# Performance work log

Measured on AMD Instinct MI355X. Metric: run time of the kernel, lower is better.

Reference implementation:

```python
import jax, jax.numpy as jnp
import numpy as np

EPS = 1e-8      # torch CosineSimilarity eps (clamps norms)
GAMMA = 0.5
RANK = 2        # hardcoded in the module; rank-1 = 1 negative per sample


def _cos_dist(a, b):
    # angular distance sqrt(2*(1-cos)) along last dim, torch-style eps on norms
    na = jnp.clip(jnp.linalg.norm(a, axis=-1), EPS)
    nb = jnp.clip(jnp.linalg.norm(b, axis=-1), EPS)
    sim = jnp.sum(a * b, axis=-1) / (na * nb)
    return jnp.sqrt(jnp.maximum(2.0 * (1.0 - sim), 1e-12))


def setup_inputs() -> dict:
    key = jax.random.key(0)
    k1, k2, k3 = jax.random.split(key, 3)
    B, D, V = 4096, 512, 50000
    return {
        "input": jax.random.normal(k1, (B, D), dtype=jnp.float32),
        "target": jax.random.normal(k2, (B, D), dtype=jnp.float32),
        "veclist": jax.random.normal(k3, (V, D), dtype=jnp.float32),
    }


def reference(input, target, veclist):
    B = input.shape[0]
    # distance to the true target per sample: [B]
    d_pos = _cos_dist(input, target)

    # brute-force angular kNN over veclist (replaces the Annoy index):
    # max cosine similarity == min angular distance
    inn = input / jnp.clip(jnp.linalg.norm(input, axis=-1, keepdims=True), EPS)
    vnn = veclist / jnp.clip(jnp.linalg.norm(veclist, axis=-1, keepdims=True), EPS)
    sims = inn @ vnn.T                                # [B, V] -- the big GEMM
    _, top_idx = jax.lax.top_k(sims, RANK)            # [B, 2]

    vec0 = veclist[top_idx[:, 0]]                     # [B, D]
    vec1 = veclist[top_idx[:, 1]]                     # [B, D]
    # skip the neighbor if it is exactly the target vector (original `torch.eq` check)
    eq0 = jnp.all(vec0 == target, axis=-1)            # [B]
    neg = jnp.where(eq0[:, None], vec1, vec0)         # [B, D]

    d_neg = _cos_dist(input, neg)                     # [B]
    # original builds sample_dist of shape [rank]=[2] (gamma_vec bug repeats gamma
    # `rank` times), with both entries identical -> sum of positives = 2*relu(margin)
    margin = GAMMA + d_pos - d_neg                    # [B]
    cost = jnp.sum(RANK * jnp.maximum(margin, 0.0))
    return cost / B
```

## Files before the change

### kernel.cpp

```cpp
#include <hip/hip_runtime.h>
#include <hip/hip_bf16.h>
#include <hip/hip_fp8.h>
#include <math.h>

#define B_ROWS 4096
#define DIMS   512
#define V_ROWS 50000
#define V_PAD  50048
#define NTILES 391
#define NT_PAD 392
#define MTILES 32
#define BKB    128
#define NROWS_ALL 54144
#define EPSF   1e-8f
#define QSCALE 64.0f
#define SCALE1 0x7F7F7F7F

typedef float f32x4 __attribute__((ext_vector_type(4)));
typedef int   i32x4 __attribute__((ext_vector_type(4)));
typedef int   i32x8 __attribute__((ext_vector_type(8)));
typedef unsigned long long u64;

__device__ __forceinline__ unsigned int pk4_fp8(float a, float b, float c, float d) {
#if __has_builtin(__builtin_amdgcn_cvt_pk_fp8_f32)
  int w = __builtin_amdgcn_cvt_pk_fp8_f32(a, b, 0, false);
  w = __builtin_amdgcn_cvt_pk_fp8_f32(c, d, w, true);
  return (unsigned int)w;
#else
  __hip_fp8_e4m3 qa(a), qb(b), qc(c), qd(d);
  return (unsigned int)qa.__x | ((unsigned int)qb.__x << 8) |
         ((unsigned int)qc.__x << 16) | ((unsigned int)qd.__x << 24);
#endif
}

__device__ __forceinline__ void lds_load16(const void* g, void* l) {
  __builtin_amdgcn_global_load_lds(
      (const __attribute__((address_space(1))) void*)g,
      (__attribute__((address_space(3))) void*)l, 16, 0, 0);
}

__device__ __forceinline__ u64 pack_key(float v, int col) {
  unsigned int u = __float_as_uint(v);
  unsigned int s = u ^ ((unsigned int)((int)u >> 31) | 0x80000000u);
  return ((u64)s << 32) | (unsigned int)(~col);
}
__device__ __forceinline__ int key_col(u64 k) {
  return (int)(~(unsigned int)k);
}
__device__ __forceinline__ void kmerge(u64& k0, u64& k1, u64 a0, u64 a1) {
  bool bt = a0 > k0;
  u64 lo = bt ? k0 : a0;
  u64 hi = bt ? a1 : k1;
  k0 = bt ? a0 : k0;
  k1 = hi > lo ? hi : lo;
}

__global__ __launch_bounds__(256)
void normalize_rows_kernel(const float* __restrict__ vsrc, const float* __restrict__ isrc,
                           unsigned char* __restrict__ vdst, unsigned char* __restrict__ idst) {
  const int l = threadIdx.x & 63;
  const int gw = (blockIdx.x * 256 + threadIdx.x) >> 6;
  const int nw = (gridDim.x * 256) >> 6;
  for (int row = gw; row < NROWS_ALL; row += nw) {
    const float* src;
    unsigned char* dst;
    if (row < V_PAD) {
      if (row >= V_ROWS) {
        *(uint2*)&vdst[(size_t)row * DIMS + l * 8] = make_uint2(0u, 0u);
        continue;
      }
      src = vsrc + (size_t)row * DIMS;
      dst = vdst + (size_t)row * DIMS;
    } else {
      src = isrc + (size_t)(row - V_PAD) * DIMS;
      dst = idst + (size_t)(row - V_PAD) * DIMS;
    }
    float4 v0 = ((const float4*)src)[l * 2];
    float4 v1 = ((const float4*)src)[l * 2 + 1];
    float ss = v0.x * v0.x + v0.y * v0.y + v0.z * v0.z + v0.w * v0.w
             + v1.x * v1.x + v1.y * v1.y + v1.z * v1.z + v1.w * v1.w;
    #pragma unroll
    for (int d = 1; d < 64; d <<= 1) ss += __shfl_xor(ss, d);
    float s = QSCALE / fmaxf(sqrtf(ss), EPSF);
    uint2 o;
    o.x = pk4_fp8(v0.x * s, v0.y * s, v0.z * s, v0.w * s);
    o.y = pk4_fp8(v1.x * s, v1.y * s, v1.z * s, v1.w * s);
    *(uint2*)&dst[l * 8] = o;
  }
}

__global__ __launch_bounds__(256, 2)
void gemm_top2_kernel(const unsigned char* __restrict__ A8,
                      const unsigned char* __restrict__ B8,
                      ulonglong2* __restrict__ cands) {
  __shared__ __align__(16) unsigned char smem[2 * 2 * 128 * BKB];

  const int bid = blockIdx.x;
  const int mt = bid & 31;
  const int nt = bid >> 5;
  const int m0 = mt * 128, n0 = nt * 128;

  const int tid = threadIdx.x;
  const int w = tid >> 6, l = tid & 63;
  const int wr = w >> 1, wc = w & 1;
  const int lq = l >> 4, lr = l & 15;
  const int h = lr & 7;

  const int s0 = ((2 * lq) ^ h) * 16;
  const int s1 = ((2 * lq + 1) ^ h) * 16;

  f32x4 acc[4][4] = {};

#define STAGE(buf, k0)                                                        \
  {                                                                           \
    unsigned char* Asb = smem + (buf) * 32768;                                \
    unsigned char* Bsb = Asb + 16384;                                         \
    _Pragma("unroll")                                                         \
    for (int it = 0; it < 4; ++it) {                                          \
      const int chunk = it * 256 + w * 64 + l;                                \
      const int row = chunk >> 3, c = chunk & 7;                              \
      const int gc = c ^ (row & 7);                                           \
      lds_load16(A8 + (size_t)(m0 + row) * DIMS + (k0) + gc * 16,             \
                 &Asb[(it * 256 + w * 64) * 16]);                             \
      lds_load16(B8 + (size_t)(n0 + row) * DIMS + (k0) + gc * 16,             \
                 &Bsb[(it * 256 + w * 64) * 16]);                             \
    }                                                                         \
  }

#define COMPUTE(buf)                                                          \
  {                                                                           \
    unsigned char* Asb = smem + (buf) * 32768;                                \
    unsigned char* Bsb = Asb + 16384;                                         \
    i32x8 bf[4];                                                              \
    _Pragma("unroll")                                                         \
    for (int tc = 0; tc < 4; ++tc) {                                          \
      const int rb = (wc * 64 + tc * 16 + lr) * BKB;                          \
      i32x4 blo = *(const i32x4*)&Bsb[rb + s0];                               \
      i32x4 bhi = *(const i32x4*)&Bsb[rb + s1];                               \
      bf[tc] = __builtin_shufflevector(blo, bhi, 0, 1, 2, 3, 4, 5, 6, 7);     \
    }                                                                         \
    _Pragma("unroll")                                                         \
    for (int tr = 0; tr < 4; ++tr) {                                          \
      const int ra = (wr * 64 + tr * 16 + lr) * BKB;                          \
      i32x4 alo = *(const i32x4*)&Asb[ra + s0];                               \
      i32x4 ahi = *(const i32x4*)&Asb[ra + s1];                               \
      i32x8 af = __builtin_shufflevector(alo, ahi, 0, 1, 2, 3, 4, 5, 6, 7);   \
      __builtin_amdgcn_s_setprio(1);                                          \
      _Pragma("unroll")                                                       \
      for (int tc = 0; tc < 4; ++tc)                                          \
        acc[tr][tc] = __builtin_amdgcn_mfma_scale_f32_16x16x128_f8f6f4(       \
            af, bf[tc], acc[tr][tc], 0, 0, 0, SCALE1, 0, SCALE1);             \
      __builtin_amdgcn_s_setprio(0);                                          \
    }                                                                         \
  }

  STAGE(0, 0);
  STAGE(1, 128);

  asm volatile("s_waitcnt vmcnt(8)" ::: "memory");
  __builtin_amdgcn_s_barrier();
  COMPUTE(0);
  __builtin_amdgcn_s_barrier();
  STAGE(0, 256);

  asm volatile("s_waitcnt vmcnt(8)" ::: "memory");
  __builtin_amdgcn_s_barrier();
  COMPUTE(1);
  __builtin_amdgcn_s_barrier();
  STAGE(1, 384);

  asm volatile("s_waitcnt vmcnt(8)" ::: "memory");
  __builtin_amdgcn_s_barrier();
  COMPUTE(0);
  __builtin_amdgcn_s_barrier();

  asm volatile("s_waitcnt vmcnt(0)" ::: "memory");
  __builtin_amdgcn_s_barrier();
  COMPUTE(1);
#undef STAGE
#undef COMPUTE

  ulonglong2 (*ep)[32] = (ulonglong2(*)[32])smem;
  const int colbase = n0 + wc * 64 + lr;

  #pragma unroll
  for (int p = 0; p < 2; ++p) {
    #pragma unroll
    for (int trh = 0; trh < 2; ++trh) {
      const int tr = p * 2 + trh;
      #pragma unroll
      for (int rg = 0; rg < 4; ++rg) {
        u64 kk[4];
        #pragma unroll
        for (int tc = 0; tc < 4; ++tc) {
          const int col = colbase + tc * 16;
          const float v = (col < V_ROWS) ? acc[tr][tc][rg] : -INFINITY;
          kk[tc] = pack_key(v, col);
        }
        const bool s01 = kk[0] > kk[1];
        u64 a0 = s01 ? kk[0] : kk[1], a1 = s01 ? kk[1] : kk[0];
        const bool s23 = kk[2] > kk[3];
        u64 b0 = s23 ? kk[2] : kk[3], b1 = s23 ? kk[3] : kk[2];
        kmerge(a0, a1, b0, b1);
        const int slot = wr * 32 + trh * 16 + lq * 4 + rg;
        ep[slot][(wc * 16 + lr) ^ (slot & 7)] = make_ulonglong2(a0, a1);
      }
    }
    __syncthreads();
    {
      const int ms = tid >> 2, q = tid & 3;
      u64 k0 = 0, k1 = 0;
      #pragma unroll
      for (int k = 0; k < 8; ++k) {
        ulonglong2 e = ep[ms][(q * 8 + k) ^ (ms & 7)];
        kmerge(k0, k1, e.x, e.y);
      }
      #pragma unroll
      for (int d = 1; d < 4; d <<= 1) {
        u64 o0 = __shfl_xor(k0, d), o1 = __shfl_xor(k1, d);
        kmerge(k0, k1, o0, o1);
      }
      if (q == 0) {
        const int row = (ms >> 5) * 64 + p * 32 + (ms & 31);
        cands[(size_t)(m0 + row) * NT_PAD + nt] = make_ulonglong2(k0, k1);
      }
    }
    __syncthreads();
  }
}

__global__ __launch_bounds__(256)
void finalize_kernel(const float* __restrict__ input, const float* __restrict__ target,
                     const float* __restrict__ veclist, const ulonglong2* __restrict__ cands,
                     float* __restrict__ contrib) {
  const int b = blockIdx.x;
  const int t = threadIdx.x;
  __shared__ ulonglong2 wpair[4];
  __shared__ int sidx[2];
  __shared__ float red[4][7];
  __shared__ int reda[4];

  u64 k0 = 0, k1 = 0;
  for (int nt = t; nt < NTILES; nt += 256) {
    ulonglong2 c = cands[(size_t)b * NT_PAD + nt];
    kmerge(k0, k1, c.x, c.y);
  }
  #pragma unroll
  for (int d = 1; d < 64; d <<= 1) {
    u64 o0 = __shfl_xor(k0, d), o1 = __shfl_xor(k1, d);
    kmerge(k0, k1, o0, o1);
  }
  if ((t & 63) == 0) wpair[t >> 6] = make_ulonglong2(k0, k1);
  __syncthreads();
  if (t == 0) {
    u64 m0k = wpair[0].x, m1k = wpair[0].y;
    for (int wd = 1; wd < 4; ++wd) kmerge(m0k, m1k, wpair[wd].x, wpair[wd].y);
    sidx[0] = key_col(m0k);
    sidx[1] = key_col(m1k);
  }
  __syncthreads();
  const int idx0 = sidx[0], idx1 = sidx[1];

  const float2* xin = (const float2*)(input  + (size_t)b * DIMS);
  const float2* xtg = (const float2*)(target + (size_t)b * DIMS);
  const float2* xv0 = (const float2*)(veclist + (size_t)idx0 * DIMS);
  const float2* xv1 = (const float2*)(veclist + (size_t)idx1 * DIMS);
  float2 xi = xin[t], tg = xtg[t], a0 = xv0[t], a1 = xv1[t];
  float s[7];
  s[0] = xi.x * xi.x + xi.y * xi.y;
  s[1] = tg.x * tg.x + tg.y * tg.y;
  s[2] = xi.x * tg.x + xi.y * tg.y;
  s[3] = a0.x * a0.x + a0.y * a0.y;
  s[4] = xi.x * a0.x + xi.y * a0.y;
  s[5] = a1.x * a1.x + a1.y * a1.y;
  s[6] = xi.x * a1.x + xi.y * a1.y;
  bool eq = (a0.x == tg.x) && (a0.y == tg.y);
  int weq = __all(eq);
  #pragma unroll
  for (int k = 0; k < 7; ++k)
    #pragma unroll
    for (int d = 1; d < 64; d <<= 1) s[k] += __shfl_xor(s[k], d);
  if ((t & 63) == 0) {
    #pragma unroll
    for (int k = 0; k < 7; ++k) red[t >> 6][k] = s[k];
    reda[t >> 6] = weq;
  }
  __syncthreads();
  if (t == 0) {
    float r[7];
    #pragma unroll
    for (int k = 0; k < 7; ++k)
      r[k] = red[0][k] + red[1][k] + red[2][k] + red[3][k];
    bool eq0 = reda[0] && reda[1] && reda[2] && reda[3];
    float na  = fmaxf(sqrtf(r[0]), EPSF);
    float ntg = fmaxf(sqrtf(r[1]), EPSF);
    float simp = r[2] / (na * ntg);
    float d_pos = sqrtf(fmaxf(2.0f * (1.0f - simp), 1e-12f));
    float nn = eq0 ? fmaxf(sqrtf(r[5]), EPSF) : fmaxf(sqrtf(r[3]), EPSF);
    float dn = eq0 ? r[6] : r[4];
    float simn = dn / (na * nn);
    float d_neg = sqrtf(fmaxf(2.0f * (1.0f - simn), 1e-12f));
    float margin = 0.5f + d_pos - d_neg;
    contrib[b] = 2.0f * fmaxf(margin, 0.0f) * (1.0f / (float)B_ROWS);
  }
}

__global__ __launch_bounds__(256)
void reduce_kernel(const float* __restrict__ contrib, float* __restrict__ out) {
  const int t = threadIdx.x;
  __shared__ float wsum[4];
  float s = 0.0f;
  for (int i = t; i < B_ROWS; i += 256) s += contrib[i];
  #pragma unroll
  for (int d = 1; d < 64; d <<= 1) s += __shfl_xor(s, d);
  if ((t & 63) == 0) wsum[t >> 6] = s;
  __syncthreads();
  if (t == 0) out[0] = wsum[0] + wsum[1] + wsum[2] + wsum[3];
}

extern "C" void kernel_launch(void* const* d_in, const int* in_sizes, int n_in,
                              void* d_out, int out_size, void* d_ws, size_t ws_size,
                              hipStream_t stream) {
  const float* input   = (const float*)d_in[0];
  const float* target  = (const float*)d_in[1];
  const float* veclist = (const float*)d_in[2];
  float* out = (float*)d_out;
  char* ws = (char*)d_ws;
  unsigned char* vnn = (unsigned char*)ws;
  unsigned char* inn = (unsigned char*)(ws + 25624576);
  ulonglong2* cands = (ulonglong2*)(ws + 27721728);
  float* contrib = (float*)(ws + 53411840);

  normalize_rows_kernel<<<4096, 256, 0, stream>>>(veclist, input, vnn, inn);
  gemm_top2_kernel<<<MTILES * NTILES, 256, 0, stream>>>(inn, vnn, cands);
  finalize_kernel<<<B_ROWS, 256, 0, stream>>>(input, target, veclist, cands, contrib);
  reduce_kernel<<<1, 256, 0, stream>>>(contrib, out);
}
```

Baseline: 362.6 us.

## Prepack A operand in MFMA fragment order and load directly to registers

The normalize kernel now writes the quantized input rows in a prepacked layout that matches the MFMA fragment order, so each lane of the GEMM can load its A fragments straight from global memory into registers and A no longer goes through LDS. LDS use per block is halved, which permits 3 blocks per CU. Block IDs are also remapped so that each XCD works on a contiguous range of N tiles, to improve L2 reuse of B. The risks are higher register pressure from holding the A fragments, global-load latency for A on the critical path, and the removal of setprio.

```diff
diff --git a/kernel.cpp b/kernel.cpp
--- a/kernel.cpp
+++ b/kernel.cpp
@@ -8,9 +8,9 @@
 #define V_ROWS 50000
 #define V_PAD  50048
 #define NTILES 391
+#define NT_VIRT 392
 #define NT_PAD 392
 #define MTILES 32
-#define BKB    128
 #define NROWS_ALL 54144
 #define EPSF   1e-8f
 #define QSCALE 64.0f
@@ -57,23 +57,20 @@
 
 __global__ __launch_bounds__(256)
 void normalize_rows_kernel(const float* __restrict__ vsrc, const float* __restrict__ isrc,
-                           unsigned char* __restrict__ vdst, unsigned char* __restrict__ idst) {
+                           unsigned char* __restrict__ vdst, unsigned char* __restrict__ apk) {
   const int l = threadIdx.x & 63;
   const int gw = (blockIdx.x * 256 + threadIdx.x) >> 6;
   const int nw = (gridDim.x * 256) >> 6;
   for (int row = gw; row < NROWS_ALL; row += nw) {
     const float* src;
-    unsigned char* dst;
     if (row < V_PAD) {
       if (row >= V_ROWS) {
         *(uint2*)&vdst[(size_t)row * DIMS + l * 8] = make_uint2(0u, 0u);
         continue;
       }
       src = vsrc + (size_t)row * DIMS;
-      dst = vdst + (size_t)row * DIMS;
     } else {
       src = isrc + (size_t)(row - V_PAD) * DIMS;
-      dst = idst + (size_t)(row - V_PAD) * DIMS;
     }
     float4 v0 = ((const float4*)src)[l * 2];
     float4 v1 = ((const float4*)src)[l * 2 + 1];
@@ -85,19 +82,30 @@
     uint2 o;
     o.x = pk4_fp8(v0.x * s, v0.y * s, v0.z * s, v0.w * s);
     o.y = pk4_fp8(v1.x * s, v1.y * s, v1.z * s, v1.w * s);
-    *(uint2*)&dst[l * 8] = o;
-  }
-}
-
-__global__ __launch_bounds__(256, 2)
-void gemm_top2_kernel(const unsigned char* __restrict__ A8,
+    if (row < V_PAD) {
+      *(uint2*)&vdst[(size_t)row * DIMS + l * 8] = o;
+    } else {
+      const int m = row - V_PAD;
+      const int rec = (((( (m >> 7) * 2 + ((m >> 6) & 1) ) * 4 + (l >> 4)) * 4
+                        + ((m >> 4) & 3)) * 2 + ((l >> 1) & 1));
+      const int off = rec * 1024 + (((l >> 2) & 3) * 16 + (m & 15)) * 16 + (l & 1) * 8;
+      *(uint2*)&apk[off] = o;
+    }
+  }
+}
+
+__global__ __launch_bounds__(256, 3)
+void gemm_top2_kernel(const unsigned char* __restrict__ Apk,
                       const unsigned char* __restrict__ B8,
                       ulonglong2* __restrict__ cands) {
-  __shared__ __align__(16) unsigned char smem[2 * 2 * 128 * BKB];
+  __shared__ __align__(16) unsigned char smem[2 * 128 * 128];
 
   const int bid = blockIdx.x;
-  const int mt = bid & 31;
-  const int nt = bid >> 5;
+  const int xcd = bid & 7;
+  const int g   = bid >> 3;
+  const int mt  = g & 31;
+  const int nt  = xcd * 49 + (g >> 5);
+  if (nt >= NTILES) return;
   const int m0 = mt * 128, n0 = nt * 128;
 
   const int tid = threadIdx.x;
@@ -109,76 +117,86 @@
   const int s0 = ((2 * lq) ^ h) * 16;
   const int s1 = ((2 * lq + 1) ^ h) * 16;
 
+  const unsigned char* const Abase =
+      Apk + (size_t)(mt * 2 + wr) * 32768 + l * 16;
+
   f32x4 acc[4][4] = {};
-
-#define STAGE(buf, k0)                                                        \
+  i32x4 areg[4][2];
+
+#define STAGEB(buf, ks)                                                       \
   {                                                                           \
-    unsigned char* Asb = smem + (buf) * 32768;                                \
-    unsigned char* Bsb = Asb + 16384;                                         \
+    unsigned char* Bsb = smem + (buf) * 16384;                                \
     _Pragma("unroll")                                                         \
     for (int it = 0; it < 4; ++it) {                                          \
-      const int chunk = it * 256 + w * 64 + l;                                \
+      const int chunk = it * 256 + w * 64 + l;                   \
       const int row = chunk >> 3, c = chunk & 7;                              \
-      const int gc = c ^ (row & 7);                                           \
-      lds_load16(A8 + (size_t)(m0 + row) * DIMS + (k0) + gc * 16,             \
-                 &Asb[(it * 256 + w * 64) * 16]);                             \
-      lds_load16(B8 + (size_t)(n0 + row) * DIMS + (k0) + gc * 16,             \
+      const int gc = c ^ (row & 7);                \
+      lds_load16(B8 + (size_t)(n0 + row) * DIMS + (ks) * 128 + gc * 16,       \
                  &Bsb[(it * 256 + w * 64) * 16]);                             \
     }                                                                         \
   }
 
+#define ALOAD(ks)                                                             \
+  {                                                                           \
+    _Pragma("unroll")                                                         \
+    for (int tr = 0; tr < 4; ++tr) {                                          \
+      areg[tr][0] = *(const i32x4*)(Abase + (ks) * 8192 + tr * 2048);         \
+      areg[tr][1] = *(const i32x4*)(Abase + (ks) * 8192 + tr * 2048 + 1024);  \
+    }                                                                         \
+  }
+
 #define COMPUTE(buf)                                                          \
   {                                                                           \
-    unsigned char* Asb = smem + (buf) * 32768;                                \
-    unsigned char* Bsb = Asb + 16384;                                         \
+    unsigned char* Bsb = smem + (buf) * 16384;                                \
     i32x8 bf[4];                                                              \
     _Pragma("unroll")                                                         \
     for (int tc = 0; tc < 4; ++tc) {                                          \
-      const int rb = (wc * 64 + tc * 16 + lr) * BKB;                          \
+      const int rb = (wc * 64 + tc * 16 + lr) * 128;                          \
       i32x4 blo = *(const i32x4*)&Bsb[rb + s0];                               \
       i32x4 bhi = *(const i32x4*)&Bsb[rb + s1];                               \
       bf[tc] = __builtin_shufflevector(blo, bhi, 0, 1, 2, 3, 4, 5, 6, 7);     \
     }                                                                         \
     _Pragma("unroll")                                                         \
     for (int tr = 0; tr < 4; ++tr) {                                          \
-      const int ra = (wr * 64 + tr * 16 + lr) * BKB;                          \
-      i32x4 alo = *(const i32x4*)&Asb[ra + s0];                               \
-      i32x4 ahi = *(const i32x4*)&Asb[ra + s1];                               \
-      i32x8 af = __builtin_shufflevector(alo, ahi, 0, 1, 2, 3, 4, 5, 6, 7);   \
-      __builtin_amdgcn_s_setprio(1);                                          \
+      i32x8 af = __builtin_shufflevector(areg[tr][0], areg[tr][1],            \
+                                         0, 1, 2, 3, 4, 5, 6, 7);             \
       _Pragma("unroll")                                                       \
       for (int tc = 0; tc < 4; ++tc)                                          \
         acc[tr][tc] = __builtin_amdgcn_mfma_scale_f32_16x16x128_f8f6f4(       \
             af, bf[tc], acc[tr][tc], 0, 0, 0, SCALE1, 0, SCALE1);             \
-      __builtin_amdgcn_s_setprio(0);                                          \
     }                                                                         \
   }
 
-  STAGE(0, 0);
-  STAGE(1, 128);
-
+#define FENCE asm volatile("" ::: "memory")
+
+  STAGEB(0, 0);
+  ALOAD(0); FENCE;
+  STAGEB(1, 1);
+  asm volatile("s_waitcnt vmcnt(4)" ::: "memory");
+  __builtin_amdgcn_s_barrier();
+  COMPUTE(0);
+  __builtin_amdgcn_s_barrier();
+  ALOAD(1); FENCE;
+  STAGEB(0, 2);
+  asm volatile("s_waitcnt vmcnt(4)" ::: "memory");
+  __builtin_amdgcn_s_barrier();
+  COMPUTE(1);
+  __builtin_amdgcn_s_barrier();
+  ALOAD(2); FENCE;
+  STAGEB(1, 3);
+  asm volatile("s_waitcnt vmcnt(4)" ::: "memory");
+  __builtin_amdgcn_s_barrier();
+  COMPUTE(0);
+  __builtin_amdgcn_s_barrier();
+  ALOAD(3); FENCE;
   asm volatile("s_waitcnt vmcnt(8)" ::: "memory");
   __builtin_amdgcn_s_barrier();
-  COMPUTE(0);
-  __builtin_amdgcn_s_barrier();
-  STAGE(0, 256);
-
-  asm volatile("s_waitcnt vmcnt(8)" ::: "memory");
-  __builtin_amdgcn_s_barrier();
   COMPUTE(1);
-  __builtin_amdgcn_s_barrier();
-  STAGE(1, 384);
-
-  asm volatile("s_waitcnt vmcnt(8)" ::: "memory");
-  __builtin_amdgcn_s_barrier();
-  COMPUTE(0);
-  __builtin_amdgcn_s_barrier();
-
-  asm volatile("s_waitcnt vmcnt(0)" ::: "memory");
-  __builtin_amdgcn_s_barrier();
-  COMPUTE(1);
-#undef STAGE
+  __syncthreads();
+#undef STAGEB
+#undef ALOAD
 #undef COMPUTE
+#undef FENCE
 
   ulonglong2 (*ep)[32] = (ulonglong2(*)[32])smem;
   const int colbase = n0 + wc * 64 + lr;
@@ -327,12 +345,12 @@
   float* out = (float*)d_out;
   char* ws = (char*)d_ws;
   unsigned char* vnn = (unsigned char*)ws;
-  unsigned char* inn = (unsigned char*)(ws + 25624576);
+  unsigned char* apk = (unsigned char*)(ws + 25624576);
   ulonglong2* cands = (ulonglong2*)(ws + 27721728);
   float* contrib = (float*)(ws + 53411840);
 
-  normalize_rows_kernel<<<4096, 256, 0, stream>>>(veclist, input, vnn, inn);
-  gemm_top2_kernel<<<MTILES * NTILES, 256, 0, stream>>>(inn, vnn, cands);
+  normalize_rows_kernel<<<4096, 256, 0, stream>>>(veclist, input, vnn, apk);
+  gemm_top2_kernel<<<NT_VIRT * MTILES, 256, 0, stream>>>(apk, vnn, cands);
   finalize_kernel<<<B_ROWS, 256, 0, stream>>>(input, target, veclist, cands, contrib);
   reduce_kernel<<<1, 256, 0, stream>>>(contrib, out);
 }
```

New measurement: 343.3 us. -5.3%, faster.
